# Kernel optimization log

Hardware: AMD Instinct MI355X
Metric: run time of the kernel (lower is better)

## Reference

```python
import jax, jax.numpy as jnp
import numpy as np

B, N, EMB, FEAT = 4, 32, 512, 512
DO = N * (N - 1) // 2  # do_num = 0.5*N*(N-1)


def _encoder(h, adj, Wt, a_src, a_dst):
    # GATencoderlayer (inferred): single-head GAT attention restricted to the
    # strictly-lower triangle so that I_A = I - attn is unit lower-triangular
    # (invertible) and causal_graph = I - I_A = attn is a nonneg. strict-lower DAG.
    feat = h @ Wt  # [B,N,F]
    scores = jax.nn.leaky_relu((feat @ a_src)[:, :, None] + (feat @ a_dst)[:, None, :], 0.2)
    strict_lower = jnp.tril(jnp.ones((N, N), dtype=bool), -1)
    mask = (adj > 0) & strict_lower
    attn = jax.nn.softmax(jnp.where(mask, scores, -1e9), axis=-1)
    attn = jnp.where(mask.any(-1, keepdims=True), attn, 0.0) * mask  # row 0 has no parents
    fU = jax.nn.relu(attn @ feat)  # [B,N,F]
    I_A = jnp.eye(N, dtype=h.dtype) - attn
    return fU, I_A[:, None]  # I_A: [B,1,N,N] (multihead=1)


def _decoder(h, W, Wt):
    # GATdecoderlayer (inferred): aggregate linearly-transformed features with the
    # provided (sampled) mixing matrix W.
    feat = h @ Wt  # [B',N,F]
    return jax.nn.relu(jnp.einsum('bij,bjf->bif', W[:, 0], feat))


def _computing(cg, eps_do, few, feb, fsw, fsb):
    # Vectorized form of the triple-nested do-calculus loops.
    # cg: [B,N,N] strictly-lower causal graph.
    Bc = cg.shape[0]
    a, b = np.triu_indices(N, 1)  # raw_do pairs, same (i<j) row-major order as the loops
    idx = np.arange(N)
    ja = idx[None, :] == a[:, None]  # [DO,N]
    jb = idx[None, :] == b[:, None]
    lower = np.tril(np.ones((N, N), dtype=bool), -1)  # j < i (loop range j<=i, i==j handled by eye)
    pos = cg > 0  # [B,N,N]
    P = (pos & jnp.asarray(lower)).astype(cg.dtype)  # parent sets pa(i) = {k<i: cg[i,k]>0}
    common = jnp.einsum('bik,bjk->bij', P, P) > 0    # pa(i) \cap pa(j) nonempty
    ja_ = ja[:, None, :]; jb_ = jb[:, None, :]       # j-axis one-hots [DO,1,N]
    ia_ = ja[:, :, None]; ib_ = jb[:, :, None]       # i-axis one-hots [DO,N,1]
    c23 = jnp.asarray(lower[None] & ((ja_ & ~ib_) | (jb_ & ~ia_)))          # [DO,N,N]
    c4 = jnp.asarray(lower[None] & ~ja_ & ~jb_ & ~ia_ & ~ib_)               # [DO,N,N]
    eye = jnp.eye(N, dtype=bool)
    label = eye[None, None] | (c23[None] & pos[:, None]) | (c4[None] & common[:, None])  # [B,DO,N,N]
    # intervened graph: zero rows a and b
    keep = jnp.asarray(~(ja | jb)).astype(cg.dtype)  # [DO,N]
    cgd = (cg[:, None] * keep[None, :, :, None]).reshape(Bc * DO, N, N) + jnp.eye(N, dtype=cg.dtype)
    I_A = jnp.linalg.inv(cgd)[:, None]  # [B*DO,1,N,N]
    e = few[0, 0] * I_A + feb[0]  # Linear(1,1) applied elementwise
    s = fsw[0, 0] * I_A + fsb[0]
    z = e + jnp.exp(0.5 * s) * eps_do  # VAE reparameterization
    W_do = jnp.where(I_A == 0, I_A, z)
    return label.reshape(Bc * DO, N, N).astype(cg.dtype), W_do


def _forward(doc_sents_h, adj, enc_Wt, enc_asrc, enc_adst, dec_Wt, fce_w, fce_b, fcs_w, fcs_b, eps_main, eps_do):
    fU, I_A = _encoder(doc_sents_h, adj, enc_Wt, enc_asrc, enc_adst)
    causal_graph = jnp.eye(N, dtype=doc_sents_h.dtype) - I_A  # [B,1,N,N]
    inv = jnp.linalg.inv(I_A)
    e = fce_w[0, 0] * inv + fce_b[0]
    s = fcs_w[0, 0] * inv + fcs_b[0]
    z = e + jnp.exp(0.5 * s) * eps_main
    W = jnp.where(inv == 0, inv, z)
    X_raw = _decoder(fU, W, dec_Wt)
    label, W_do = _computing(causal_graph[:, 0], eps_do, fce_w, fce_b, fcs_w, fcs_b)
    h_do = jnp.broadcast_to(fU[:, None], (B, DO, N, FEAT)).reshape(B * DO, N, FEAT)
    X_do = _decoder(h_do, W_do, dec_Wt)
    return X_raw, X_do, label, causal_graph, e, s


def setup_inputs():
    key = jax.random.key(0)
    ks = jax.random.split(key, 10)
    return {
        'doc_sents_h': jax.random.normal(ks[0], (B, N, EMB), jnp.float32) * 0.5,
        'adj': jnp.ones((B, N, N), jnp.float32),
        'doc_len': jnp.full((B,), N, jnp.int32),
        'enc_Wt': jax.random.normal(ks[1], (EMB, FEAT), jnp.float32) / np.sqrt(EMB).astype(np.float32),
        'enc_asrc': jax.random.normal(ks[2], (FEAT,), jnp.float32) * 0.1,
        'enc_adst': jax.random.normal(ks[3], (FEAT,), jnp.float32) * 0.1,
        'dec_Wt': jax.random.normal(ks[4], (FEAT, FEAT), jnp.float32) / np.sqrt(FEAT).astype(np.float32),
        'fce_w': jax.random.normal(ks[5], (1, 1), jnp.float32) * 0.1,
        'fce_b': jax.random.normal(ks[6], (1,), jnp.float32) * 0.1,
        'fcs_w': jax.random.normal(ks[7], (1, 1), jnp.float32) * 0.1,
        'fcs_b': jax.random.normal(ks[8], (1,), jnp.float32) * 0.1,
        'eps_main': jax.random.normal(ks[9], (B, 1, N, N), jnp.float32),
        'eps_do': jax.random.normal(jax.random.fold_in(key, 1), (B * DO, 1, N, N), jnp.float32),
    }


def reference(doc_sents_h, adj, doc_len, enc_Wt, enc_asrc, enc_adst, dec_Wt, fce_w, fce_b, fcs_w, fcs_b, eps_main, eps_do):
    del doc_len  # original only asserts max(doc_len) == max_doc_len
    return _forward(doc_sents_h, adj, enc_Wt, enc_asrc, enc_adst, dec_Wt, fce_w, fce_b, fcs_w, fcs_b, eps_main, eps_do)
```

## Files before the change

### kernel.cpp

```cpp
#include <hip/hip_runtime.h>
#include <math.h>

#define N 32
#define B 4
#define EMB 512
#define FEAT 512
#define NDO 496
#define BDO (B*NDO)

#define OFF_XRAW  ((size_t)0)
#define OFF_XDO   ((size_t)(B*N*FEAT))
#define OFF_LABEL (OFF_XDO + (size_t)BDO*N*FEAT)
#define OFF_CG    (OFF_LABEL + (size_t)BDO*N*N)
#define OFF_E     (OFF_CG + (size_t)B*N*N)
#define OFF_S     (OFF_E + (size_t)B*N*N)

#define WS_FEAT   0
#define WS_SRC    (WS_FEAT + B*N*FEAT)
#define WS_DST    (WS_SRC + B*N)
#define WS_ATTN   (WS_DST + B*N)
#define WS_W      (WS_ATTN + B*N*N)
#define WS_FU     (WS_W + B*N*N)
#define WS_FEAT2  (WS_FU + B*N*FEAT)
#define WS_POS    (WS_FEAT2 + B*N*FEAT)
#define WS_COM    (WS_POS + B*N)

template<bool WITH_ATT>
__global__ __launch_bounds__(128) void rowgemm_kernel(
    const float* __restrict__ X, const float* __restrict__ Wt,
    float* __restrict__ out,
    const float* __restrict__ a_src, const float* __restrict__ a_dst,
    float* __restrict__ src_out, float* __restrict__ dst_out)
{
    __shared__ float xrow[512];
    __shared__ float red[2][2];
    const int row = blockIdx.x;
    const int tid = threadIdx.x;
    reinterpret_cast<float4*>(xrow)[tid] =
        reinterpret_cast<const float4*>(X + (size_t)row * 512)[tid];
    __syncthreads();
    const int c = tid * 4;
    float a0 = 0.f, a1 = 0.f, a2 = 0.f, a3 = 0.f;
    for (int k = 0; k < 512; ++k) {
        const float hv = xrow[k];
        const float4 w = *reinterpret_cast<const float4*>(Wt + (size_t)k * 512 + c);
        a0 = fmaf(hv, w.x, a0); a1 = fmaf(hv, w.y, a1);
        a2 = fmaf(hv, w.z, a2); a3 = fmaf(hv, w.w, a3);
    }
    *reinterpret_cast<float4*>(out + (size_t)row * 512 + c) = make_float4(a0, a1, a2, a3);
    if (WITH_ATT) {
        const float4 as = *reinterpret_cast<const float4*>(a_src + c);
        const float4 ad = *reinterpret_cast<const float4*>(a_dst + c);
        float ps = a0 * as.x + a1 * as.y + a2 * as.z + a3 * as.w;
        float pd = a0 * ad.x + a1 * ad.y + a2 * ad.z + a3 * ad.w;
        #pragma unroll
        for (int off = 32; off > 0; off >>= 1) {
            ps += __shfl_down(ps, off);
            pd += __shfl_down(pd, off);
        }
        const int wave = tid >> 6;
        if ((tid & 63) == 0) { red[wave][0] = ps; red[wave][1] = pd; }
        __syncthreads();
        if (tid == 0) {
            src_out[row] = red[0][0] + red[1][0];
            dst_out[row] = red[0][1] + red[1][1];
        }
    }
}

__global__ __launch_bounds__(256) void batch_kernel(
    const float* __restrict__ adj, const float* __restrict__ featp,
    const float* __restrict__ srcp, const float* __restrict__ dstp,
    const float* __restrict__ fce_w, const float* __restrict__ fce_b,
    const float* __restrict__ fcs_w, const float* __restrict__ fcs_b,
    const float* __restrict__ eps_main,
    float* __restrict__ out,
    float* __restrict__ ws_attn, float* __restrict__ ws_W,
    float* __restrict__ ws_fU,
    unsigned* __restrict__ posb, unsigned* __restrict__ comb)
{
    __shared__ float attnL[N * N];
    __shared__ float Minv[N * N];
    __shared__ float dstL[N];
    __shared__ unsigned pbits[N];
    const int b = blockIdx.x;
    const int tid = threadIdx.x;
    if (tid < N) dstL[tid] = dstp[b * N + tid];
    __syncthreads();
    if (tid < N) {
        const int i = tid;
        const float srcv = srcp[b * N + i];
        const float* arow = adj + (size_t)b * N * N + i * N;
        float sc[N];
        float mx = -3e38f;
        bool any = false;
        #pragma unroll
        for (int j = 0; j < N; ++j) {
            const bool m = (arow[j] > 0.f) && (j < i);
            float x = srcv + dstL[j];
            x = (x >= 0.f) ? x : 0.2f * x;
            sc[j] = m ? x : -3e38f;
            if (m) { any = true; mx = fmaxf(mx, x); }
        }
        float den = 0.f;
        #pragma unroll
        for (int j = 0; j < N; ++j) {
            const float e = (sc[j] > -1e38f) ? __expf(sc[j] - mx) : 0.f;
            sc[j] = e;
            den += e;
        }
        const float inv_den = any ? (1.f / den) : 0.f;
        unsigned pb = 0;
        #pragma unroll
        for (int j = 0; j < N; ++j) {
            const float a = sc[j] * inv_den;
            attnL[i * N + j] = a;
            if (a > 0.f) pb |= (1u << j);
        }
        pbits[i] = pb;
        posb[b * N + i] = pb;
    }
    __syncthreads();
    for (int idx = tid; idx < N * N; idx += 256) {
        const float a = attnL[idx];
        out[OFF_CG + (size_t)b * N * N + idx] = a;
        ws_attn[b * N * N + idx] = a;
    }
    if (tid < N) {
        const unsigned my = pbits[tid];
        unsigned cb = 0;
        #pragma unroll
        for (int j = 0; j < N; ++j) if (my & pbits[j]) cb |= (1u << j);
        comb[b * N + tid] = cb;
    }
    if (tid < N) {
        const int j = tid;
        float x[N];
        #pragma unroll
        for (int i = 0; i < N; ++i) {
            float s = (i == j) ? 1.f : 0.f;
            #pragma unroll
            for (int k = 0; k < N; ++k)
                if (k < i) s = fmaf(attnL[i * N + k], x[k], s);
            x[i] = s;
            Minv[i * N + j] = s;
        }
    }
    __syncthreads();
    const float few = fce_w[0], feb = fce_b[0], fsw = fcs_w[0], fsb = fcs_b[0];
    for (int idx = tid; idx < N * N; idx += 256) {
        const float m = Minv[idx];
        const float e = fmaf(few, m, feb);
        const float s2 = fmaf(fsw, m, fsb);
        out[OFF_E + (size_t)b * N * N + idx] = e;
        out[OFF_S + (size_t)b * N * N + idx] = s2;
        ws_W[b * N * N + idx] = (m == 0.f) ? 0.f
            : fmaf(__expf(0.5f * s2), eps_main[b * N * N + idx], e);
    }
    const int c = 2 * tid;
    float2 v[N];
    #pragma unroll
    for (int j = 0; j < N; ++j)
        v[j] = *reinterpret_cast<const float2*>(&featp[(size_t)(b * N + j) * FEAT + c]);
    #pragma unroll
    for (int i = 0; i < N; ++i) {
        float s0 = 0.f, s1 = 0.f;
        #pragma unroll
        for (int j4 = 0; j4 < 8; ++j4) {
            if (4 * j4 < i) {
                const float4 w = *reinterpret_cast<const float4*>(&attnL[i * N + 4 * j4]);
                s0 = fmaf(w.x, v[4*j4+0].x, s0); s1 = fmaf(w.x, v[4*j4+0].y, s1);
                s0 = fmaf(w.y, v[4*j4+1].x, s0); s1 = fmaf(w.y, v[4*j4+1].y, s1);
                s0 = fmaf(w.z, v[4*j4+2].x, s0); s1 = fmaf(w.z, v[4*j4+2].y, s1);
                s0 = fmaf(w.w, v[4*j4+3].x, s0); s1 = fmaf(w.w, v[4*j4+3].y, s1);
            }
        }
        *reinterpret_cast<float2*>(&ws_fU[(size_t)(b * N + i) * FEAT + c]) =
            make_float2(fmaxf(s0, 0.f), fmaxf(s1, 0.f));
    }
}

__global__ __launch_bounds__(128) void xraw_kernel(
    const float* __restrict__ ws_W, const float* __restrict__ ws_feat2,
    float* __restrict__ out)
{
    const int row = blockIdx.x;
    const int b = row >> 5, i = row & 31;
    __shared__ float Wrow[N];
    const int tid = threadIdx.x;
    if (tid < N) Wrow[tid] = ws_W[(size_t)b * N * N + i * N + tid];
    __syncthreads();
    const int c = 4 * tid;
    float4 acc = make_float4(0.f, 0.f, 0.f, 0.f);
    #pragma unroll
    for (int j = 0; j < N; ++j) {
        const float w = Wrow[j];
        const float4 f = *reinterpret_cast<const float4*>(&ws_feat2[(size_t)(b * N + j) * FEAT + c]);
        acc.x = fmaf(w, f.x, acc.x); acc.y = fmaf(w, f.y, acc.y);
        acc.z = fmaf(w, f.z, acc.z); acc.w = fmaf(w, f.w, acc.w);
    }
    *reinterpret_cast<float4*>(&out[OFF_XRAW + (size_t)row * FEAT + c]) =
        make_float4(fmaxf(acc.x, 0.f), fmaxf(acc.y, 0.f), fmaxf(acc.z, 0.f), fmaxf(acc.w, 0.f));
}

__global__ __launch_bounds__(256) void do_kernel(
    const float* __restrict__ ws_attn, const float* __restrict__ ws_feat2,
    const unsigned* __restrict__ posb, const unsigned* __restrict__ comb,
    const float* __restrict__ fce_w, const float* __restrict__ fce_b,
    const float* __restrict__ fcs_w, const float* __restrict__ fcs_b,
    const float* __restrict__ eps_do,
    float* __restrict__ out)
{
    __shared__ float L[N * N];
    __shared__ float Minv[N * N];
    __shared__ float Wd[N * N];
    const int p = blockIdx.x;
    const int b = p / NDO;
    int tt = p - b * NDO;
    int ai = 0, rem = N - 1;
    while (tt >= rem) { tt -= rem; ++ai; --rem; }
    const int bi = ai + 1 + tt;
    const int tid = threadIdx.x;
    for (int idx = tid; idx < N * N; idx += 256) {
        const int i = idx >> 5;
        const float vv = ws_attn[b * N * N + idx];
        L[idx] = (i == ai || i == bi) ? 0.f : vv;
    }
    const int c = 2 * tid;
    float2 v[N];
    #pragma unroll
    for (int j = 0; j < N; ++j)
        v[j] = *reinterpret_cast<const float2*>(&ws_feat2[(size_t)(b * N + j) * FEAT + c]);
    __syncthreads();
    if (tid < N) {
        const int j = tid;
        float x[N];
        #pragma unroll
        for (int i = 0; i < N; ++i) {
            float s = (i == j) ? 1.f : 0.f;
            #pragma unroll
            for (int k = 0; k < N; ++k)
                if (k < i) s = fmaf(-L[i * N + k], x[k], s);
            x[i] = s;
            Minv[i * N + j] = s;
        }
    }
    __syncthreads();
    const float few = fce_w[0], feb = fce_b[0], fsw = fcs_w[0], fsb = fcs_b[0];
    for (int idx = tid; idx < N * N; idx += 256) {
        const int i = idx >> 5, j = idx & 31;
        const float m = Minv[idx];
        const float e = fmaf(few, m, feb);
        const float s2 = fmaf(fsw, m, fsb);
        Wd[idx] = (m == 0.f) ? 0.f
            : fmaf(__expf(0.5f * s2), eps_do[(size_t)p * N * N + idx], e);
        const bool lower = i > j;
        const bool c23 = lower && (((j == ai) && (i != bi)) || ((j == bi) && (i != ai)));
        const bool c4 = lower && (i != ai) && (i != bi) && (j != ai) && (j != bi);
        const bool pos = (posb[b * N + i] >> j) & 1u;
        const bool com = (comb[b * N + i] >> j) & 1u;
        const bool lab = (i == j) || (c23 && pos) || (c4 && com);
        out[OFF_LABEL + (size_t)p * N * N + idx] = lab ? 1.f : 0.f;
    }
    __syncthreads();
    float* Xdo = out + OFF_XDO + (size_t)p * N * FEAT;
    #pragma unroll
    for (int i = 0; i < N; ++i) {
        float s0 = 0.f, s1 = 0.f;
        #pragma unroll
        for (int j4 = 0; j4 < 8; ++j4) {
            if (4 * j4 <= i) {
                const float4 w = *reinterpret_cast<const float4*>(&Wd[i * N + 4 * j4]);
                s0 = fmaf(w.x, v[4*j4+0].x, s0); s1 = fmaf(w.x, v[4*j4+0].y, s1);
                s0 = fmaf(w.y, v[4*j4+1].x, s0); s1 = fmaf(w.y, v[4*j4+1].y, s1);
                s0 = fmaf(w.z, v[4*j4+2].x, s0); s1 = fmaf(w.z, v[4*j4+2].y, s1);
                s0 = fmaf(w.w, v[4*j4+3].x, s0); s1 = fmaf(w.w, v[4*j4+3].y, s1);
            }
        }
        *reinterpret_cast<float2*>(&Xdo[(size_t)i * FEAT + c]) =
            make_float2(fmaxf(s0, 0.f), fmaxf(s1, 0.f));
    }
}

extern "C" void kernel_launch(void* const* d_in, const int* in_sizes, int n_in,
                              void* d_out, int out_size, void* d_ws, size_t ws_size,
                              hipStream_t stream)
{
    const float* h        = (const float*)d_in[0];
    const float* adj      = (const float*)d_in[1];
    const float* enc_Wt   = (const float*)d_in[3];
    const float* a_src    = (const float*)d_in[4];
    const float* a_dst    = (const float*)d_in[5];
    const float* dec_Wt   = (const float*)d_in[6];
    const float* fce_w    = (const float*)d_in[7];
    const float* fce_b    = (const float*)d_in[8];
    const float* fcs_w    = (const float*)d_in[9];
    const float* fcs_b    = (const float*)d_in[10];
    const float* eps_main = (const float*)d_in[11];
    const float* eps_do   = (const float*)d_in[12];
    float* out = (float*)d_out;
    float* ws  = (float*)d_ws;

    float* ws_feat  = ws + WS_FEAT;
    float* ws_src   = ws + WS_SRC;
    float* ws_dst   = ws + WS_DST;
    float* ws_attn  = ws + WS_ATTN;
    float* ws_W     = ws + WS_W;
    float* ws_fU    = ws + WS_FU;
    float* ws_feat2 = ws + WS_FEAT2;
    unsigned* ws_pos = (unsigned*)(ws + WS_POS);
    unsigned* ws_com = (unsigned*)(ws + WS_COM);

    rowgemm_kernel<true><<<B * N, 128, 0, stream>>>(
        h, enc_Wt, ws_feat, a_src, a_dst, ws_src, ws_dst);
    batch_kernel<<<B, 256, 0, stream>>>(
        adj, ws_feat, ws_src, ws_dst, fce_w, fce_b, fcs_w, fcs_b,
        eps_main, out, ws_attn, ws_W, ws_fU, ws_pos, ws_com);
    rowgemm_kernel<false><<<B * N, 128, 0, stream>>>(
        ws_fU, dec_Wt, ws_feat2, nullptr, nullptr, nullptr, nullptr);
    xraw_kernel<<<B * N, 128, 0, stream>>>(ws_W, ws_feat2, out);
    do_kernel<<<BDO, 256, 0, stream>>>(
        ws_attn, ws_feat2, ws_pos, ws_com, fce_w, fce_b, fcs_w, fcs_b,
        eps_do, out);
}
```

Measured before the change: 109.1 us.

## Retile row GEMMs, move attention projections into batch kernel, vectorize do_kernel

The row GEMM now gives each block four input rows and a 64-column chunk, splits K across two waves and reduces through shared memory. Each weight load is reused across four rows and the grid grows to 256 blocks. The src/dst attention projections move from the GEMM epilogue into batch_kernel, which computes them from the stored features. do_kernel loads eps and labels as float4 up front and splits the output columns into two 256-wide halves to cut register pressure, at the cost of a second pass over Wd.

After: 113.6 us. +4.1%, slower.

```diff
diff --git a/kernel.cpp b/kernel.cpp
--- a/kernel.cpp
+++ b/kernel.cpp
@@ -16,61 +16,54 @@
 #define OFF_S     (OFF_E + (size_t)B*N*N)
 
 #define WS_FEAT   0
-#define WS_SRC    (WS_FEAT + B*N*FEAT)
-#define WS_DST    (WS_SRC + B*N)
-#define WS_ATTN   (WS_DST + B*N)
+#define WS_ATTN   (WS_FEAT + B*N*FEAT)
 #define WS_W      (WS_ATTN + B*N*N)
 #define WS_FU     (WS_W + B*N*N)
 #define WS_FEAT2  (WS_FU + B*N*FEAT)
 #define WS_POS    (WS_FEAT2 + B*N*FEAT)
 #define WS_COM    (WS_POS + B*N)
 
-template<bool WITH_ATT>
-__global__ __launch_bounds__(128) void rowgemm_kernel(
+__global__ __launch_bounds__(128) void rowgemm4_kernel(
     const float* __restrict__ X, const float* __restrict__ Wt,
-    float* __restrict__ out,
-    const float* __restrict__ a_src, const float* __restrict__ a_dst,
-    float* __restrict__ src_out, float* __restrict__ dst_out)
-{
-    __shared__ float xrow[512];
-    __shared__ float red[2][2];
-    const int row = blockIdx.x;
+    float* __restrict__ out)
+{
+    __shared__ __align__(16) float ht[512][4];
+    __shared__ __align__(16) float red[64 * 4];
+    const int rg  = blockIdx.x >> 3;
+    const int ch  = blockIdx.x & 7;
     const int tid = threadIdx.x;
-    reinterpret_cast<float4*>(xrow)[tid] =
-        reinterpret_cast<const float4*>(X + (size_t)row * 512)[tid];
-    __syncthreads();
-    const int c = tid * 4;
+    const int c   = tid & 63;
+    const int kh  = tid >> 6;
+    for (int idx = tid; idx < 2048; idx += 128) {
+        const int r = idx >> 9, k = idx & 511;
+        ht[k][r] = X[(size_t)(rg * 4 + r) * 512 + k];
+    }
+    __syncthreads();
     float a0 = 0.f, a1 = 0.f, a2 = 0.f, a3 = 0.f;
-    for (int k = 0; k < 512; ++k) {
-        const float hv = xrow[k];
-        const float4 w = *reinterpret_cast<const float4*>(Wt + (size_t)k * 512 + c);
-        a0 = fmaf(hv, w.x, a0); a1 = fmaf(hv, w.y, a1);
-        a2 = fmaf(hv, w.z, a2); a3 = fmaf(hv, w.w, a3);
-    }
-    *reinterpret_cast<float4*>(out + (size_t)row * 512 + c) = make_float4(a0, a1, a2, a3);
-    if (WITH_ATT) {
-        const float4 as = *reinterpret_cast<const float4*>(a_src + c);
-        const float4 ad = *reinterpret_cast<const float4*>(a_dst + c);
-        float ps = a0 * as.x + a1 * as.y + a2 * as.z + a3 * as.w;
-        float pd = a0 * ad.x + a1 * ad.y + a2 * ad.z + a3 * ad.w;
-        #pragma unroll
-        for (int off = 32; off > 0; off >>= 1) {
-            ps += __shfl_down(ps, off);
-            pd += __shfl_down(pd, off);
-        }
-        const int wave = tid >> 6;
-        if ((tid & 63) == 0) { red[wave][0] = ps; red[wave][1] = pd; }
-        __syncthreads();
-        if (tid == 0) {
-            src_out[row] = red[0][0] + red[1][0];
-            dst_out[row] = red[0][1] + red[1][1];
-        }
+    const float* wp = Wt + (size_t)(kh * 256) * 512 + ch * 64 + c;
+    const float4* hp = reinterpret_cast<const float4*>(&ht[kh * 256][0]);
+    #pragma unroll 8
+    for (int k = 0; k < 256; ++k) {
+        const float w = wp[(size_t)k * 512];
+        const float4 h4 = hp[k];
+        a0 = fmaf(w, h4.x, a0); a1 = fmaf(w, h4.y, a1);
+        a2 = fmaf(w, h4.z, a2); a3 = fmaf(w, h4.w, a3);
+    }
+    if (kh) *reinterpret_cast<float4*>(&red[c * 4]) = make_float4(a0, a1, a2, a3);
+    __syncthreads();
+    if (!kh) {
+        const float4 r4 = *reinterpret_cast<const float4*>(&red[c * 4]);
+        const size_t base = (size_t)(rg * 4) * 512 + ch * 64 + c;
+        out[base]            = a0 + r4.x;
+        out[base + 512]      = a1 + r4.y;
+        out[base + 1024]     = a2 + r4.z;
+        out[base + 1536]     = a3 + r4.w;
     }
 }
 
 __global__ __launch_bounds__(256) void batch_kernel(
     const float* __restrict__ adj, const float* __restrict__ featp,
-    const float* __restrict__ srcp, const float* __restrict__ dstp,
+    const float* __restrict__ a_src, const float* __restrict__ a_dst,
     const float* __restrict__ fce_w, const float* __restrict__ fce_b,
     const float* __restrict__ fcs_w, const float* __restrict__ fcs_b,
     const float* __restrict__ eps_main,
@@ -81,15 +74,33 @@
 {
     __shared__ float attnL[N * N];
     __shared__ float Minv[N * N];
-    __shared__ float dstL[N];
+    __shared__ float srcS[N], dstS[N];
     __shared__ unsigned pbits[N];
     const int b = blockIdx.x;
     const int tid = threadIdx.x;
-    if (tid < N) dstL[tid] = dstp[b * N + tid];
+    {
+        const int row = tid >> 3, seg = tid & 7;
+        const float* fp = featp + (size_t)(b * N + row) * 512 + seg * 64;
+        const float* as = a_src + seg * 64;
+        const float* ad = a_dst + seg * 64;
+        float ps = 0.f, pd = 0.f;
+        #pragma unroll
+        for (int q = 0; q < 16; ++q) {
+            const float4 f  = reinterpret_cast<const float4*>(fp)[q];
+            const float4 s4 = reinterpret_cast<const float4*>(as)[q];
+            const float4 d4 = reinterpret_cast<const float4*>(ad)[q];
+            ps += f.x * s4.x + f.y * s4.y + f.z * s4.z + f.w * s4.w;
+            pd += f.x * d4.x + f.y * d4.y + f.z * d4.z + f.w * d4.w;
+        }
+        ps += __shfl_down(ps, 4); pd += __shfl_down(pd, 4);
+        ps += __shfl_down(ps, 2); pd += __shfl_down(pd, 2);
+        ps += __shfl_down(ps, 1); pd += __shfl_down(pd, 1);
+        if ((tid & 7) == 0) { srcS[row] = ps; dstS[row] = pd; }
+    }
     __syncthreads();
     if (tid < N) {
         const int i = tid;
-        const float srcv = srcp[b * N + i];
+        const float srcv = srcS[i];
         const float* arow = adj + (size_t)b * N * N + i * N;
         float sc[N];
         float mx = -3e38f;
@@ -97,7 +108,7 @@
         #pragma unroll
         for (int j = 0; j < N; ++j) {
             const bool m = (arow[j] > 0.f) && (j < i);
-            float x = srcv + dstL[j];
+            float x = srcv + dstS[j];
             x = (x >= 0.f) ? x : 0.2f * x;
             sc[j] = m ? x : -3e38f;
             if (m) { any = true; mx = fmaxf(mx, x); }
@@ -221,16 +232,33 @@
     while (tt >= rem) { tt -= rem; ++ai; --rem; }
     const int bi = ai + 1 + tt;
     const int tid = threadIdx.x;
-    for (int idx = tid; idx < N * N; idx += 256) {
-        const int i = idx >> 5;
-        const float vv = ws_attn[b * N * N + idx];
-        L[idx] = (i == ai || i == bi) ? 0.f : vv;
-    }
-    const int c = 2 * tid;
-    float2 v[N];
+    const int i0 = tid >> 3;
+    const int j0 = (tid & 7) * 4;
+    float4 lv = *reinterpret_cast<const float4*>(&ws_attn[(size_t)b * N * N + 4 * tid]);
+    if (i0 == ai || i0 == bi) lv = make_float4(0.f, 0.f, 0.f, 0.f);
+    *reinterpret_cast<float4*>(&L[4 * tid]) = lv;
+    const float4 ev = *reinterpret_cast<const float4*>(&eps_do[(size_t)p * N * N + 4 * tid]);
+    {
+        const unsigned pb = posb[b * N + i0];
+        const unsigned cb = comb[b * N + i0];
+        float4 lab;
+        float* lp = &lab.x;
+        #pragma unroll
+        for (int q = 0; q < 4; ++q) {
+            const int j = j0 + q;
+            const bool lower = i0 > j;
+            const bool c23 = lower && (((j == ai) && (i0 != bi)) || ((j == bi) && (i0 != ai)));
+            const bool c4 = lower && (i0 != ai) && (i0 != bi) && (j != ai) && (j != bi);
+            const bool pos = (pb >> j) & 1u;
+            const bool com = (cb >> j) & 1u;
+            lp[q] = ((i0 == j) || (c23 && pos) || (c4 && com)) ? 1.f : 0.f;
+        }
+        *reinterpret_cast<float4*>(&out[OFF_LABEL + (size_t)p * N * N + 4 * tid]) = lab;
+    }
+    float v0[N];
     #pragma unroll
     for (int j = 0; j < N; ++j)
-        v[j] = *reinterpret_cast<const float2*>(&ws_feat2[(size_t)(b * N + j) * FEAT + c]);
+        v0[j] = ws_feat2[(size_t)(b * N + j) * FEAT + tid];
     __syncthreads();
     if (tid < N) {
         const int j = tid;
@@ -247,38 +275,56 @@
     }
     __syncthreads();
     const float few = fce_w[0], feb = fce_b[0], fsw = fcs_w[0], fsb = fcs_b[0];
-    for (int idx = tid; idx < N * N; idx += 256) {
-        const int i = idx >> 5, j = idx & 31;
-        const float m = Minv[idx];
-        const float e = fmaf(few, m, feb);
-        const float s2 = fmaf(fsw, m, fsb);
-        Wd[idx] = (m == 0.f) ? 0.f
-            : fmaf(__expf(0.5f * s2), eps_do[(size_t)p * N * N + idx], e);
-        const bool lower = i > j;
-        const bool c23 = lower && (((j == ai) && (i != bi)) || ((j == bi) && (i != ai)));
-        const bool c4 = lower && (i != ai) && (i != bi) && (j != ai) && (j != bi);
-        const bool pos = (posb[b * N + i] >> j) & 1u;
-        const bool com = (comb[b * N + i] >> j) & 1u;
-        const bool lab = (i == j) || (c23 && pos) || (c4 && com);
-        out[OFF_LABEL + (size_t)p * N * N + idx] = lab ? 1.f : 0.f;
+    {
+        const float4 m4 = *reinterpret_cast<const float4*>(&Minv[4 * tid]);
+        const float* mp = &m4.x;
+        const float* ep = &ev.x;
+        float4 w4;
+        float* wp = &w4.x;
+        #pragma unroll
+        for (int q = 0; q < 4; ++q) {
+            const float m = mp[q];
+            const float e = fmaf(few, m, feb);
+            const float s2 = fmaf(fsw, m, fsb);
+            wp[q] = (m == 0.f) ? 0.f : fmaf(__expf(0.5f * s2), ep[q], e);
+        }
+        *reinterpret_cast<float4*>(&Wd[4 * tid]) = w4;
     }
     __syncthreads();
     float* Xdo = out + OFF_XDO + (size_t)p * N * FEAT;
+    float v1[N];
+    #pragma unroll
+    for (int j = 0; j < N; ++j)
+        v1[j] = ws_feat2[(size_t)(b * N + j) * FEAT + 256 + tid];
     #pragma unroll
     for (int i = 0; i < N; ++i) {
-        float s0 = 0.f, s1 = 0.f;
+        float s = 0.f;
         #pragma unroll
         for (int j4 = 0; j4 < 8; ++j4) {
             if (4 * j4 <= i) {
                 const float4 w = *reinterpret_cast<const float4*>(&Wd[i * N + 4 * j4]);
-                s0 = fmaf(w.x, v[4*j4+0].x, s0); s1 = fmaf(w.x, v[4*j4+0].y, s1);
-                s0 = fmaf(w.y, v[4*j4+1].x, s0); s1 = fmaf(w.y, v[4*j4+1].y, s1);
-                s0 = fmaf(w.z, v[4*j4+2].x, s0); s1 = fmaf(w.z, v[4*j4+2].y, s1);
-                s0 = fmaf(w.w, v[4*j4+3].x, s0); s1 = fmaf(w.w, v[4*j4+3].y, s1);
+                s = fmaf(w.x, v0[4*j4+0], s);
+                s = fmaf(w.y, v0[4*j4+1], s);
+                s = fmaf(w.z, v0[4*j4+2], s);
+                s = fmaf(w.w, v0[4*j4+3], s);
             }
         }
-        *reinterpret_cast<float2*>(&Xdo[(size_t)i * FEAT + c]) =
-            make_float2(fmaxf(s0, 0.f), fmaxf(s1, 0.f));
+        Xdo[(size_t)i * FEAT + tid] = fmaxf(s, 0.f);
+    }
+    #pragma unroll
+    for (int i = 0; i < N; ++i) {
+        float s = 0.f;
+        #pragma unroll
+        for (int j4 = 0; j4 < 8; ++j4) {
+            if (4 * j4 <= i) {
+                const float4 w = *reinterpret_cast<const float4*>(&Wd[i * N + 4 * j4]);
+                s = fmaf(w.x, v1[4*j4+0], s);
+                s = fmaf(w.y, v1[4*j4+1], s);
+                s = fmaf(w.z, v1[4*j4+2], s);
+                s = fmaf(w.w, v1[4*j4+3], s);
+            }
+        }
+        Xdo[(size_t)i * FEAT + 256 + tid] = fmaxf(s, 0.f);
     }
 }
 
@@ -302,8 +348,6 @@
     float* ws  = (float*)d_ws;
 
     float* ws_feat  = ws + WS_FEAT;
-    float* ws_src   = ws + WS_SRC;
-    float* ws_dst   = ws + WS_DST;
     float* ws_attn  = ws + WS_ATTN;
     float* ws_W     = ws + WS_W;
     float* ws_fU    = ws + WS_FU;
@@ -311,13 +355,11 @@
     unsigned* ws_pos = (unsigned*)(ws + WS_POS);
     unsigned* ws_com = (unsigned*)(ws + WS_COM);
 
-    rowgemm_kernel<true><<<B * N, 128, 0, stream>>>(
-        h, enc_Wt, ws_feat, a_src, a_dst, ws_src, ws_dst);
+    rowgemm4_kernel<<<256, 128, 0, stream>>>(h, enc_Wt, ws_feat);
     batch_kernel<<<B, 256, 0, stream>>>(
-        adj, ws_feat, ws_src, ws_dst, fce_w, fce_b, fcs_w, fcs_b,
+        adj, ws_feat, a_src, a_dst, fce_w, fce_b, fcs_w, fcs_b,
         eps_main, out, ws_attn, ws_W, ws_fU, ws_pos, ws_com);
-    rowgemm_kernel<false><<<B * N, 128, 0, stream>>>(
-        ws_fU, dec_Wt, ws_feat2, nullptr, nullptr, nullptr, nullptr);
+    rowgemm4_kernel<<<256, 128, 0, stream>>>(ws_fU, dec_Wt, ws_feat2);
     xraw_kernel<<<B * N, 128, 0, stream>>>(ws_W, ws_feat2, out);
     do_kernel<<<BDO, 256, 0, stream>>>(
         ws_attn, ws_feat2, ws_pos, ws_com, fce_w, fce_b, fcs_w, fcs_b,
```
